# Kernel optimization log

Hardware: AMD Instinct MI355X
Metric: run time of the kernel (lower is better)

Reference implementation:

```python
import jax, jax.numpy as jnp
import numpy as np

N, D = 8192, 256
EPS = 1e-12  # guards sqrt(0) on the diagonal


def setup_inputs() -> dict:
    key = jax.random.key(0)
    kx, = jax.random.split(key, 1)
    x = jax.random.normal(kx, (N, D), dtype=jnp.float32)
    threshold = jnp.zeros((1,), dtype=jnp.float32)  # nn.Parameter(torch.zeros(1))
    t = jnp.ones((1,), dtype=jnp.float32)           # nn.Parameter(torch.ones(1))
    return {"x": x, "threshold": threshold, "t": t}


def reference(x, threshold, t):
    # Sigmoid-like branch: pairwise euclidean distance without materializing [N,N,D].
    # |x_i - x_j|^2 summed over D == ||x_i||^2 + ||x_j||^2 - 2 x_i.x_j  (abs is a no-op under squaring)
    sq = jnp.sum(x * x, axis=1)  # [N]
    dist2 = sq[:, None] + sq[None, :] - 2.0 * (x @ x.T)  # [N, N]
    dist = jnp.sqrt(jnp.maximum(dist2, EPS))
    diff = (dist + threshold) * t  # broadcast scalar params
    return 1.0 - jax.nn.sigmoid(diff)
```

## Files before the change

### kernel.cpp

```cpp
#include <hip/hip_runtime.h>
#include <cstdint>
#include <cstddef>

#define NN 8192
#define DD 256

typedef __bf16 bf16x8 __attribute__((ext_vector_type(8)));
typedef float f32x4 __attribute__((ext_vector_type(4)));
typedef unsigned short ushort8 __attribute__((ext_vector_type(8)));

__global__ __launch_bounds__(256) void prep_kernel(const float* __restrict__ x,
                                                   unsigned short* __restrict__ xbt,
                                                   float* __restrict__ sq) {
    const int t = threadIdx.x;
    const int oct = t & 31;
    const int rl = t >> 5;
    const int row = blockIdx.x * 8 + rl;
    const float4* xp = (const float4*)(x + (size_t)row * DD + oct * 8);
    const float4 a = xp[0], b = xp[1];
    const float vs[8] = {a.x, a.y, a.z, a.w, b.x, b.y, b.z, b.w};
    ushort8 o;
    float p = 0.0f;
#pragma unroll
    for (int i = 0; i < 8; ++i) {
        const float v = vs[i];
        const unsigned int u = __float_as_uint(v);
        o[i] = (unsigned short)((u + 0x7FFFu + ((u >> 16) & 1u)) >> 16);
        p = fmaf(v, v, p);
    }
    *(ushort8*)(xbt + ((size_t)oct * NN + row) * 8) = o;
#pragma unroll
    for (int off = 16; off > 0; off >>= 1) p += __shfl_down(p, off, 32);
    if (oct == 0) sq[row] = p;
}

__global__ __launch_bounds__(256) void gemm_sig_kernel(
    const unsigned short* __restrict__ XbT, const float* __restrict__ sq,
    const float* __restrict__ thrp, const float* __restrict__ tp,
    float* __restrict__ out) {
    const int tid = threadIdx.x;
    const int wave = tid >> 6;
    const int lane = tid & 63;

    const int brow = blockIdx.y;
    const int bcol = blockIdx.x;
    const int wrow = (wave >> 1) * 64;
    const int wcol = (wave & 1) * 64;

    const int fr = lane & 15;
    const int q = lane >> 4;

    const size_t rowA0 = (size_t)brow * 128;
    const size_t rowB0 = (size_t)bcol * 128;

    const unsigned short* pA = XbT + ((size_t)q * NN + rowA0 + wrow + fr) * 8;
    const unsigned short* pB = XbT + ((size_t)q * NN + rowB0 + wcol + fr) * 8;
    const size_t kkStride = (size_t)4 * NN * 8;

    f32x4 acc[4][4] = {};
    bf16x8 afp[2][4], bfp[2][4];

#pragma unroll
    for (int t = 0; t < 4; ++t) {
        afp[0][t] = *(const bf16x8*)(pA + t * 128);
        bfp[0][t] = *(const bf16x8*)(pB + t * 128);
    }
#pragma unroll
    for (int kk = 0; kk < 8; ++kk) {
        const int cur = kk & 1, nxt = cur ^ 1;
        if (kk < 7) {
            const unsigned short* nA = pA + (size_t)(kk + 1) * kkStride;
            const unsigned short* nB = pB + (size_t)(kk + 1) * kkStride;
#pragma unroll
            for (int t = 0; t < 4; ++t) {
                afp[nxt][t] = *(const bf16x8*)(nA + t * 128);
                bfp[nxt][t] = *(const bf16x8*)(nB + t * 128);
            }
        }
#pragma unroll
        for (int ti = 0; ti < 4; ++ti)
#pragma unroll
            for (int tj = 0; tj < 4; ++tj)
                acc[ti][tj] = __builtin_amdgcn_mfma_f32_16x16x32_bf16(
                    afp[cur][ti], bfp[cur][tj], acc[ti][tj], 0, 0, 0);
    }

    const float tv = tp[0];
    const float thr_t = thrp[0] * tv;
    const int c0 = lane & 15;
    const int r0q = (lane >> 4) * 4;

    float sqi[16], sqj[4];
#pragma unroll
    for (int ti = 0; ti < 4; ++ti)
#pragma unroll
        for (int rg = 0; rg < 4; ++rg)
            sqi[ti * 4 + rg] = sq[rowA0 + wrow + ti * 16 + r0q + rg];
#pragma unroll
    for (int tj = 0; tj < 4; ++tj) sqj[tj] = sq[rowB0 + wcol + tj * 16 + c0];

    float* ob = out + (rowA0 + wrow + r0q) * NN + (rowB0 + wcol + c0);

    if (brow != bcol) {
#pragma unroll
        for (int ti = 0; ti < 4; ++ti)
#pragma unroll
            for (int tj = 0; tj < 4; ++tj)
#pragma unroll
                for (int rg = 0; rg < 4; ++rg) {
                    float d2 = fmaf(-2.0f, acc[ti][tj][rg], sqi[ti * 4 + rg] + sqj[tj]);
                    d2 = fmaxf(d2, 1e-12f);
                    const float dist = __builtin_amdgcn_sqrtf(d2);
                    const float e = __expf(fmaf(dist, tv, thr_t));
                    ob[(size_t)(ti * 16 + rg) * NN + tj * 16] =
                        __builtin_amdgcn_rcpf(1.0f + e);
                }
    } else {
#pragma unroll
        for (int ti = 0; ti < 4; ++ti)
#pragma unroll
            for (int tj = 0; tj < 4; ++tj)
#pragma unroll
                for (int rg = 0; rg < 4; ++rg) {
                    const int rloc = wrow + ti * 16 + r0q + rg;
                    const int cloc = wcol + tj * 16 + c0;
                    float d2 = fmaf(-2.0f, acc[ti][tj][rg], sqi[ti * 4 + rg] + sqj[tj]);
                    if (rloc == cloc) d2 = 0.0f;
                    d2 = fmaxf(d2, 1e-12f);
                    const float dist = __builtin_amdgcn_sqrtf(d2);
                    const float e = __expf(fmaf(dist, tv, thr_t));
                    ob[(size_t)(ti * 16 + rg) * NN + tj * 16] =
                        __builtin_amdgcn_rcpf(1.0f + e);
                }
    }
}

extern "C" void kernel_launch(void* const* d_in, const int* in_sizes, int n_in,
                              void* d_out, int out_size, void* d_ws, size_t ws_size,
                              hipStream_t stream) {
    const float* x = (const float*)d_in[0];
    const float* threshold = (const float*)d_in[1];
    const float* t = (const float*)d_in[2];
    float* out = (float*)d_out;

    unsigned short* xbt = (unsigned short*)d_ws;
    float* sq = (float*)((char*)d_ws + (size_t)NN * DD * sizeof(unsigned short));

    prep_kernel<<<NN / 8, 256, 0, stream>>>(x, xbt, sq);
    dim3 grid(NN / 128, NN / 128);
    gemm_sig_kernel<<<grid, 256, 0, stream>>>(xbt, sq, threshold, t, out);
}
```

Measured before the change: 299.2 us.

## Switch GEMM to 32x32x16 MFMA with 32-bit offsets and occupancy hint

Replaces the 4x4 grid of 16x16x32 bf16 MFMAs per wave with a 2x2 grid of 32x32x16 MFMAs. This halves the number of fragment loads per k-step and uses the larger-tile instruction, which has higher throughput per issue. Address arithmetic moves to 32-bit offsets, and __launch_bounds__(256,4) asks for higher occupancy. The diagonal-block branch is folded into a per-element row==col check, which adds a compare to every output element.

```diff
diff --git a/kernel.cpp b/kernel.cpp
--- a/kernel.cpp
+++ b/kernel.cpp
@@ -6,7 +6,7 @@
 #define DD 256
 
 typedef __bf16 bf16x8 __attribute__((ext_vector_type(8)));
-typedef float f32x4 __attribute__((ext_vector_type(4)));
+typedef float f32x16 __attribute__((ext_vector_type(16)));
 typedef unsigned short ushort8 __attribute__((ext_vector_type(8)));
 
 __global__ __launch_bounds__(256) void prep_kernel(const float* __restrict__ x,
@@ -34,104 +34,81 @@
     if (oct == 0) sq[row] = p;
 }
 
-__global__ __launch_bounds__(256) void gemm_sig_kernel(
+__global__ __launch_bounds__(256, 4) void gemm_sig_kernel(
     const unsigned short* __restrict__ XbT, const float* __restrict__ sq,
     const float* __restrict__ thrp, const float* __restrict__ tp,
     float* __restrict__ out) {
     const int tid = threadIdx.x;
     const int wave = tid >> 6;
     const int lane = tid & 63;
+    const int m = lane & 31;
+    const int q2 = lane >> 5;
 
     const int brow = blockIdx.y;
     const int bcol = blockIdx.x;
     const int wrow = (wave >> 1) * 64;
     const int wcol = (wave & 1) * 64;
 
-    const int fr = lane & 15;
-    const int q = lane >> 4;
+    const uint32_t rowA0 = (uint32_t)brow * 128;
+    const uint32_t rowB0 = (uint32_t)bcol * 128;
 
-    const size_t rowA0 = (size_t)brow * 128;
-    const size_t rowB0 = (size_t)bcol * 128;
+    const uint32_t offA = ((uint32_t)q2 * NN + rowA0 + wrow + m) * 8;
+    const uint32_t offB = ((uint32_t)q2 * NN + rowB0 + wcol + m) * 8;
+    const uint32_t kkS = 2u * NN * 8;
 
-    const unsigned short* pA = XbT + ((size_t)q * NN + rowA0 + wrow + fr) * 8;
-    const unsigned short* pB = XbT + ((size_t)q * NN + rowB0 + wcol + fr) * 8;
-    const size_t kkStride = (size_t)4 * NN * 8;
-
-    f32x4 acc[4][4] = {};
-    bf16x8 afp[2][4], bfp[2][4];
+    f32x16 acc[2][2] = {};
+    bf16x8 af[2][2], bfv[2][2];
 
 #pragma unroll
-    for (int t = 0; t < 4; ++t) {
-        afp[0][t] = *(const bf16x8*)(pA + t * 128);
-        bfp[0][t] = *(const bf16x8*)(pB + t * 128);
+    for (int t = 0; t < 2; ++t) {
+        af[0][t]  = *(const bf16x8*)(XbT + offA + t * 256);
+        bfv[0][t] = *(const bf16x8*)(XbT + offB + t * 256);
     }
 #pragma unroll
-    for (int kk = 0; kk < 8; ++kk) {
+    for (int kk = 0; kk < 16; ++kk) {
         const int cur = kk & 1, nxt = cur ^ 1;
-        if (kk < 7) {
-            const unsigned short* nA = pA + (size_t)(kk + 1) * kkStride;
-            const unsigned short* nB = pB + (size_t)(kk + 1) * kkStride;
+        if (kk < 15) {
+            const uint32_t ko = (uint32_t)(kk + 1) * kkS;
 #pragma unroll
-            for (int t = 0; t < 4; ++t) {
-                afp[nxt][t] = *(const bf16x8*)(nA + t * 128);
-                bfp[nxt][t] = *(const bf16x8*)(nB + t * 128);
+            for (int t = 0; t < 2; ++t) {
+                af[nxt][t]  = *(const bf16x8*)(XbT + offA + ko + t * 256);
+                bfv[nxt][t] = *(const bf16x8*)(XbT + offB + ko + t * 256);
             }
         }
 #pragma unroll
-        for (int ti = 0; ti < 4; ++ti)
+        for (int ti = 0; ti < 2; ++ti)
 #pragma unroll
-            for (int tj = 0; tj < 4; ++tj)
-                acc[ti][tj] = __builtin_amdgcn_mfma_f32_16x16x32_bf16(
-                    afp[cur][ti], bfp[cur][tj], acc[ti][tj], 0, 0, 0);
+            for (int tj = 0; tj < 2; ++tj)
+                acc[ti][tj] = __builtin_amdgcn_mfma_f32_32x32x16_bf16(
+                    af[cur][ti], bfv[cur][tj], acc[ti][tj], 0, 0, 0);
     }
 
     const float tv = tp[0];
     const float thr_t = thrp[0] * tv;
-    const int c0 = lane & 15;
-    const int r0q = (lane >> 4) * 4;
+    const uint32_t colg0 = rowB0 + wcol + m;
 
-    float sqi[16], sqj[4];
 #pragma unroll
-    for (int ti = 0; ti < 4; ++ti)
+    for (int ti = 0; ti < 2; ++ti) {
+        const uint32_t rbase = rowA0 + wrow + ti * 32 + 4 * q2;
+        float sqi[16];
 #pragma unroll
-        for (int rg = 0; rg < 4; ++rg)
-            sqi[ti * 4 + rg] = sq[rowA0 + wrow + ti * 16 + r0q + rg];
+        for (int rg = 0; rg < 16; ++rg)
+            sqi[rg] = sq[rbase + (rg & 3) + 8 * (rg >> 2)];
 #pragma unroll
-    for (int tj = 0; tj < 4; ++tj) sqj[tj] = sq[rowB0 + wcol + tj * 16 + c0];
-
-    float* ob = out + (rowA0 + wrow + r0q) * NN + (rowB0 + wcol + c0);
-
-    if (brow != bcol) {
+        for (int tj = 0; tj < 2; ++tj) {
+            const uint32_t colg = colg0 + tj * 32;
+            const float sqj = sq[colg];
 #pragma unroll
-        for (int ti = 0; ti < 4; ++ti)
-#pragma unroll
-            for (int tj = 0; tj < 4; ++tj)
-#pragma unroll
-                for (int rg = 0; rg < 4; ++rg) {
-                    float d2 = fmaf(-2.0f, acc[ti][tj][rg], sqi[ti * 4 + rg] + sqj[tj]);
-                    d2 = fmaxf(d2, 1e-12f);
-                    const float dist = __builtin_amdgcn_sqrtf(d2);
-                    const float e = __expf(fmaf(dist, tv, thr_t));
-                    ob[(size_t)(ti * 16 + rg) * NN + tj * 16] =
-                        __builtin_amdgcn_rcpf(1.0f + e);
-                }
-    } else {
-#pragma unroll
-        for (int ti = 0; ti < 4; ++ti)
-#pragma unroll
-            for (int tj = 0; tj < 4; ++tj)
-#pragma unroll
-                for (int rg = 0; rg < 4; ++rg) {
-                    const int rloc = wrow + ti * 16 + r0q + rg;
-                    const int cloc = wcol + tj * 16 + c0;
-                    float d2 = fmaf(-2.0f, acc[ti][tj][rg], sqi[ti * 4 + rg] + sqj[tj]);
-                    if (rloc == cloc) d2 = 0.0f;
-                    d2 = fmaxf(d2, 1e-12f);
-                    const float dist = __builtin_amdgcn_sqrtf(d2);
-                    const float e = __expf(fmaf(dist, tv, thr_t));
-                    ob[(size_t)(ti * 16 + rg) * NN + tj * 16] =
-                        __builtin_amdgcn_rcpf(1.0f + e);
-                }
+            for (int rg = 0; rg < 16; ++rg) {
+                const uint32_t r = rbase + (rg & 3) + 8 * (rg >> 2);
+                float d2 = fmaf(-2.0f, acc[ti][tj][rg], sqi[rg] + sqj);
+                if (r == colg) d2 = 0.0f;
+                d2 = fmaxf(d2, 1e-12f);
+                const float dist = __builtin_amdgcn_sqrtf(d2);
+                const float e = __expf(fmaf(dist, tv, thr_t));
+                out[(size_t)r * NN + colg] = __builtin_amdgcn_rcpf(1.0f + e);
+            }
+        }
     }
 }
 
```

New measurement: 286.8 us. 1.04x faster.
